# Kernel optimization log

Measured on AMD Instinct MI355X. Metric: run time of the kernel, lower is better.

Reference implementation:

```python
import jax, jax.numpy as jnp
import numpy as np

IN_CAPS, IN_DIMS = 32, 288
OUT_CAPS, OUT_DIMS = 10, 16
N_ITERS = 3


def setup_inputs() -> dict:
    key = jax.random.key(0)
    k1, k2 = jax.random.split(key)
    B = 8192
    data = jax.random.normal(k1, (B, IN_CAPS, IN_DIMS), dtype=jnp.float32)
    stdv = 1.0 / 32.0
    W = jax.random.uniform(k2, (IN_CAPS, IN_DIMS, OUT_CAPS * OUT_DIMS),
                           dtype=jnp.float32, minval=-stdv, maxval=stdv)
    return {"data": data, "W": W}


def reference(data, W):
    B = data.shape[0]
    # u_hat[b,i,o,d]: per-input-capsule predictions for each output capsule
    u_hat = jnp.einsum('bci,cio->bco', data, W).reshape(B, IN_CAPS, OUT_CAPS, OUT_DIMS)
    b = jnp.zeros((IN_CAPS, OUT_CAPS), dtype=u_hat.dtype)
    v = None
    for _ in range(N_ITERS):  # fixed small iteration count
        c = jax.nn.softmax(b, axis=0)                      # (IN_CAPS, OUT_CAPS), softmax over input capsules
        v = jnp.einsum('io,biod->bod', c, u_hat)           # (B, OUT_CAPS, OUT_DIMS)
        # agreement: sqrt of sum of squared elementwise products, averaged over batch
        a = jnp.sqrt(jnp.sum((u_hat * v[:, None, :, :]) ** 2, axis=-1)).mean(axis=0)
        b = b + a
    return v
```

## Files before the change

### kernel.cpp

```cpp
#include <hip/hip_runtime.h>
#include <hip/hip_bf16.h>

#define NB 8192
#define IC 32
#define ID 288
#define OD16 160

typedef __attribute__((ext_vector_type(8))) short bf16x8;
typedef __attribute__((ext_vector_type(4))) float f32x4;

__device__ __forceinline__ unsigned short f2bf(float f) {
    unsigned int u = __builtin_bit_cast(unsigned int, f);
    u = u + 0x7fffu + ((u >> 16) & 1u);
    return (unsigned short)(u >> 16);
}
__device__ __forceinline__ float bf2f(unsigned short h) {
    return __builtin_bit_cast(float, ((unsigned int)h) << 16);
}
__device__ __forceinline__ bf16x8 cvt_bf8(const float4& a, const float4& b) {
    union { __hip_bfloat162 h[4]; bf16x8 v; } u;
    u.h[0] = __float22bfloat162_rn(make_float2(a.x, a.y));
    u.h[1] = __float22bfloat162_rn(make_float2(a.z, a.w));
    u.h[2] = __float22bfloat162_rn(make_float2(b.x, b.y));
    u.h[3] = __float22bfloat162_rn(make_float2(b.z, b.w));
    return u.v;
}

__device__ __forceinline__ void gld_lds16(const void* g, void* l) {
    __builtin_amdgcn_global_load_lds((const __attribute__((address_space(1))) unsigned int*)g,
                                     (__attribute__((address_space(3))) unsigned int*)l, 16, 0, 0);
}

__global__ __launch_bounds__(256) void prep_kernel(const float* __restrict__ W,
                                                   unsigned short* __restrict__ WtImg,
                                                   float* __restrict__ a_arr) {
    __shared__ short tile[160 * 72];
    const int bx = blockIdx.x;
    const int c = bx / 5;
    const int s = bx - c * 5;
    const int t = threadIdx.x;
    if (bx == 0) {
        for (int i = t; i < 3 * 8 * 320; i += 256) a_arr[i] = 0.f;
    }
    const int kw = (s == 4) ? 32 : 64;
    const int nel = kw * 160;
    for (int idx = t; idx < nel; idx += 256) {
        int k = idx / 160;
        int n = idx - k * 160;
        tile[n * 72 + k] = (short)f2bf(W[((long)c * ID + s * 64 + k) * OD16 + n]);
    }
    __syncthreads();
    unsigned short* dst = WtImg + ((long)c * 5 + s) * 10240;
    for (int p = t; p < 1280; p += 256) {
        int n = p >> 3;
        int g = (p & 7) ^ (n & 7);
        uint4 val = make_uint4(0u, 0u, 0u, 0u);
        if (g * 8 < kw) val = *(const uint4*)&tile[n * 72 + g * 8];
        *(uint4*)(dst + p * 8) = val;
    }
}

__global__ __launch_bounds__(256) void gemm_kernel(const float* __restrict__ data,
                                                   const unsigned short* __restrict__ WtImg,
                                                   unsigned short* __restrict__ uhat) {
    __shared__ alignas(16) char Bb[2][20480];
    const int tid = threadIdx.x;
    const int lane = tid & 63;
    const int w = tid >> 6;
    const int q = lane >> 4;
    const int r = lane & 15;
    const int b0 = blockIdx.x * 128;
    const int cc = blockIdx.y;

    const float* A0 = data + (long)(b0 + w * 32 + r) * (IC * ID) + cc * ID;
    const float* A1 = A0 + 16 * (IC * ID);
    const unsigned short* Wc = WtImg + (long)cc * 51200;

    f32x4 acc[2][10];
    #pragma unroll
    for (int i = 0; i < 2; ++i)
        #pragma unroll
        for (int j = 0; j < 10; ++j)
            acc[i][j] = (f32x4){0.f, 0.f, 0.f, 0.f};

    float4 av[2][2][2][2];

    auto issueB = [&](int buf, int s) {
        const unsigned short* src = Wc + s * 10240 + (w * 5) * 512 + lane * 8;
        char* dst = &Bb[buf][(w * 5) * 1024];
        #pragma unroll
        for (int j = 0; j < 5; ++j)
            gld_lds16(src + j * 512, dst + j * 1024);
    };

#define ISSUEA(BANK, S, NKC)                                                   \
    {                                                                          \
        _Pragma("unroll")                                                      \
        for (int kc = 0; kc < (NKC); ++kc) {                                   \
            const int k = (S) * 64 + kc * 32 + q * 8;                          \
            av[BANK][0][kc][0] = *(const float4*)(A0 + k);                     \
            av[BANK][0][kc][1] = *(const float4*)(A0 + k + 4);                 \
            av[BANK][1][kc][0] = *(const float4*)(A1 + k);                     \
            av[BANK][1][kc][1] = *(const float4*)(A1 + k + 4);                 \
        }                                                                      \
    }

#define COMPUTE(BANK, CUR, NKC)                                                \
    {                                                                          \
        _Pragma("unroll")                                                      \
        for (int kc = 0; kc < (NKC); ++kc) {                                   \
            const int kb = kc * 64 + q * 16;                                   \
            bf16x8 bfr[10];                                                    \
            _Pragma("unroll")                                                  \
            for (int nf = 0; nf < 10; ++nf) {                                  \
                const int n = nf * 16 + r;                                     \
                bfr[nf] = *(const bf16x8*)(&Bb[CUR][(n * 128 + kb) ^ ((n & 7) << 4)]); \
            }                                                                  \
            bf16x8 af0 = cvt_bf8(av[BANK][0][kc][0], av[BANK][0][kc][1]);      \
            bf16x8 af1 = cvt_bf8(av[BANK][1][kc][0], av[BANK][1][kc][1]);      \
            _Pragma("unroll")                                                  \
            for (int nf = 0; nf < 10; ++nf) {                                  \
                acc[0][nf] = __builtin_amdgcn_mfma_f32_16x16x32_bf16(af0, bfr[nf], acc[0][nf], 0, 0, 0); \
                acc[1][nf] = __builtin_amdgcn_mfma_f32_16x16x32_bf16(af1, bfr[nf], acc[1][nf], 0, 0, 0); \
            }                                                                  \
        }                                                                      \
    }

#define STAGE(S, BANK, CUR, NKC, NKC_NEXT, WAIT)                               \
    {                                                                          \
        if ((S) < 4) { ISSUEA(1 - (BANK), (S) + 1, NKC_NEXT); issueB(1 - (CUR), (S) + 1); } \
        asm volatile("s_waitcnt vmcnt(" WAIT ")" ::: "memory");                \
        __builtin_amdgcn_s_barrier();                                          \
        __builtin_amdgcn_sched_barrier(0);                                     \
        COMPUTE(BANK, CUR, NKC);                                               \
        if ((S) < 4) __builtin_amdgcn_s_barrier();                             \
    }

    ISSUEA(0, 0, 2);
    issueB(0, 0);

    STAGE(0, 0, 0, 2, 2, "13")
    STAGE(1, 1, 1, 2, 2, "13")
    STAGE(2, 0, 0, 2, 2, "13")
    STAGE(3, 1, 1, 2, 1, "9")
    STAGE(4, 0, 0, 1, 0, "0")

#undef STAGE
#undef COMPUTE
#undef ISSUEA

    __syncthreads();
    short* eb = (short*)&Bb[0][0];
    #pragma unroll
    for (int mf = 0; mf < 2; ++mf)
        #pragma unroll
        for (int rr = 0; rr < 4; ++rr) {
            const int m = w * 32 + mf * 16 + (q << 2) + rr;
            #pragma unroll
            for (int nf = 0; nf < 10; ++nf)
                eb[m * 160 + nf * 16 + r] = (short)f2bf(acc[mf][nf][rr]);
        }
    __syncthreads();
    unsigned short* dstc = uhat + ((long)cc * NB + b0) * 160;
    #pragma unroll
    for (int j = 0; j < 10; ++j) {
        const int chunk = j * 256 + tid;
        *(uint4*)(dstc + chunk * 8) = *(const uint4*)(eb + chunk * 8);
    }
}

template <int COMPUTE_A, int WRITE_V>
__global__ __launch_bounds__(256) void route_kernel(const unsigned short* __restrict__ uhat,
                                                    const float* __restrict__ a_all,
                                                    int n_prev,
                                                    float* __restrict__ a_out,
                                                    float* __restrict__ v_out) {
    constexpr long PL = (long)NB * 160;
    __shared__ float c_sh[320];
    __shared__ float v_lds[4][160];
    __shared__ float a_sh[4][320];
    const int tid = threadIdx.x;
    for (int base = 0; base < 320; base += 256) {
        int t = base + tid;
        if (t < 320) {
            float bv = 0.f;
            for (int j = 0; j < n_prev * 8; ++j) bv += a_all[j * 320 + t];
            bv *= (1.0f / 8192.0f);
            float m = bv;
            #pragma unroll
            for (int off = 1; off < 32; off <<= 1) m = fmaxf(m, __shfl_xor(m, off));
            float e = __expf(bv - m);
            float ssum = e;
            #pragma unroll
            for (int off = 1; off < 32; off <<= 1) ssum += __shfl_xor(ssum, off);
            c_sh[t] = e / ssum;
        }
    }
    __syncthreads();

    const int w = tid >> 6;
    const int lane = tid & 63;
    const long row = (long)blockIdx.x * 4 + w;
    const unsigned short* __restrict__ u = uhat + row * 160;

    ushort4 ua[5][4];
    if (COMPUTE_A) {
        #pragma unroll
        for (int s5 = 0; s5 < 5; ++s5) {
            const int i = lane & 31;
            const int oo = (lane >> 5) + 2 * s5;
            #pragma unroll
            for (int d4 = 0; d4 < 4; ++d4)
                ua[s5][d4] = *(const ushort4*)(u + (long)i * PL + oo * 16 + d4 * 4);
        }
    }

    if (lane < 40) {
        const int q = lane;
        const int o = q >> 2;
        float4 sv = {0.f, 0.f, 0.f, 0.f};
        #pragma unroll 8
        for (int i = 0; i < 32; ++i) {
            ushort4 uu = *(const ushort4*)(u + (long)i * PL + q * 4);
            float ci = c_sh[o * 32 + i];
            sv.x += ci * bf2f(uu.x);
            sv.y += ci * bf2f(uu.y);
            sv.z += ci * bf2f(uu.z);
            sv.w += ci * bf2f(uu.w);
        }
        if (WRITE_V) *(float4*)(v_out + row * 160 + q * 4) = sv;
        if (COMPUTE_A) *(float4*)(&v_lds[w][q * 4]) = sv;
    }

    if (COMPUTE_A) {
        asm volatile("s_waitcnt lgkmcnt(0)" ::: "memory");
        #pragma unroll
        for (int s5 = 0; s5 < 5; ++s5) {
            const int i = lane & 31;
            const int oo = (lane >> 5) + 2 * s5;
            const float* vp = &v_lds[w][oo * 16];
            float accv = 0.f;
            #pragma unroll
            for (int d4 = 0; d4 < 4; ++d4) {
                ushort4 uu = ua[s5][d4];
                float4 vv = *(const float4*)(vp + d4 * 4);
                float p0 = bf2f(uu.x) * vv.x;
                float p1 = bf2f(uu.y) * vv.y;
                float p2 = bf2f(uu.z) * vv.z;
                float p3 = bf2f(uu.w) * vv.w;
                accv += p0 * p0 + p1 * p1 + p2 * p2 + p3 * p3;
            }
            a_sh[w][oo * 32 + i] = sqrtf(accv);
        }
        __syncthreads();
        for (int t = tid; t < 320; t += 256) {
            float s4 = a_sh[0][t] + a_sh[1][t] + a_sh[2][t] + a_sh[3][t];
            atomicAdd(a_out + (blockIdx.x & 7) * 320 + t, s4);
        }
    }
}

extern "C" void kernel_launch(void* const* d_in, const int* in_sizes, int n_in,
                              void* d_out, int out_size, void* d_ws, size_t ws_size,
                              hipStream_t stream) {
    const float* data = (const float*)d_in[0];
    const float* W = (const float*)d_in[1];
    float* out = (float*)d_out;
    char* ws = (char*)d_ws;

    unsigned short* uhat = (unsigned short*)ws;
    size_t off = (size_t)NB * IC * OD16 * 2;
    unsigned short* WtImg = (unsigned short*)(ws + off);
    off += 32L * 5 * 10240 * 2;
    float* a_arr = (float*)(ws + off); off += 3 * 8 * 320 * 4;

    hipLaunchKernelGGL(prep_kernel, dim3(160), dim3(256), 0, stream, W, WtImg, a_arr);
    hipLaunchKernelGGL(gemm_kernel, dim3(64, 32), dim3(256), 0, stream, data, WtImg, uhat);
    hipLaunchKernelGGL((route_kernel<1, 0>), dim3(2048), dim3(256), 0, stream,
                       uhat, a_arr, 0, a_arr + 0 * 2560, out);
    hipLaunchKernelGGL((route_kernel<1, 0>), dim3(2048), dim3(256), 0, stream,
                       uhat, a_arr, 1, a_arr + 1 * 2560, out);
    hipLaunchKernelGGL((route_kernel<0, 1>), dim3(2048), dim3(256), 0, stream,
                       uhat, a_arr, 2, a_arr + 2 * 2560, out);
}
```

Baseline: 194.2 us.

## Stage A operand through LDS via async global_load_lds with swizzled layout

The fp32 activation tile (A) now goes through LDS with async global_load_lds, using an XOR-swizzled layout per wave, instead of being loaded into registers. The main loop is restructured into nine k-chunk computes, with separate double buffering for A and B and hand-placed vmcnt waits and barriers. The aim is to cut register pressure from the register prefetch and to overlap global loads more deeply with MFMA work. In exchange, LDS use grows to 72KB per block, which can lower occupancy, and each k-chunk adds extra LDS reads.

```diff
diff --git a/kernel.cpp b/kernel.cpp
--- a/kernel.cpp
+++ b/kernel.cpp
@@ -17,12 +17,12 @@
 __device__ __forceinline__ float bf2f(unsigned short h) {
     return __builtin_bit_cast(float, ((unsigned int)h) << 16);
 }
-__device__ __forceinline__ bf16x8 cvt_bf8(const float4& a, const float4& b) {
+__device__ __forceinline__ bf16x8 cvt_bf8(const f32x4& a, const f32x4& b) {
     union { __hip_bfloat162 h[4]; bf16x8 v; } u;
-    u.h[0] = __float22bfloat162_rn(make_float2(a.x, a.y));
-    u.h[1] = __float22bfloat162_rn(make_float2(a.z, a.w));
-    u.h[2] = __float22bfloat162_rn(make_float2(b.x, b.y));
-    u.h[3] = __float22bfloat162_rn(make_float2(b.z, b.w));
+    u.h[0] = __float22bfloat162_rn(make_float2(a[0], a[1]));
+    u.h[1] = __float22bfloat162_rn(make_float2(a[2], a[3]));
+    u.h[2] = __float22bfloat162_rn(make_float2(b[0], b[1]));
+    u.h[3] = __float22bfloat162_rn(make_float2(b[2], b[3]));
     return u.v;
 }
 
@@ -63,7 +63,9 @@
 __global__ __launch_bounds__(256) void gemm_kernel(const float* __restrict__ data,
                                                    const unsigned short* __restrict__ WtImg,
                                                    unsigned short* __restrict__ uhat) {
-    __shared__ alignas(16) char Bb[2][20480];
+    __shared__ alignas(16) char lds[73728];
+    char* const Alds = lds;
+    char* const Blds = lds + 32768;
     const int tid = threadIdx.x;
     const int lane = tid & 63;
     const int w = tid >> 6;
@@ -72,8 +74,8 @@
     const int b0 = blockIdx.x * 128;
     const int cc = blockIdx.y;
 
-    const float* A0 = data + (long)(b0 + w * 32 + r) * (IC * ID) + cc * ID;
-    const float* A1 = A0 + 16 * (IC * ID);
+    const float* Ag = data + (long)(b0 + w * 32 + (lane >> 3)) * (IC * ID) + cc * ID
+                      + ((lane & 7) ^ ((lane >> 3) & 7)) * 4;
     const unsigned short* Wc = WtImg + (long)cc * 51200;
 
     f32x4 acc[2][10];
@@ -83,74 +85,70 @@
         for (int j = 0; j < 10; ++j)
             acc[i][j] = (f32x4){0.f, 0.f, 0.f, 0.f};
 
-    float4 av[2][2][2][2];
-
+    auto issueA = [&](int buf, int kc) {
+        char* dst = Alds + w * 8192 + buf * 4096;
+        const float* src = Ag + kc * 32;
+        #pragma unroll
+        for (int j = 0; j < 4; ++j)
+            gld_lds16(src + (long)j * 8 * (IC * ID), dst + j * 1024);
+    };
     auto issueB = [&](int buf, int s) {
         const unsigned short* src = Wc + s * 10240 + (w * 5) * 512 + lane * 8;
-        char* dst = &Bb[buf][(w * 5) * 1024];
+        char* dst = Blds + buf * 20480 + (w * 5) * 1024;
         #pragma unroll
         for (int j = 0; j < 5; ++j)
             gld_lds16(src + j * 512, dst + j * 1024);
     };
 
-#define ISSUEA(BANK, S, NKC)                                                   \
+#define COMPUTE(KC)                                                            \
     {                                                                          \
+        const char* Ab = Alds + w * 8192 + ((KC) & 1) * 4096;                  \
+        const char* Bb = Blds + (((KC) >> 1) & 1) * 20480;                     \
+        const int kb = ((KC) & 1) * 64 + q * 16;                               \
+        bf16x8 bfr[10];                                                        \
         _Pragma("unroll")                                                      \
-        for (int kc = 0; kc < (NKC); ++kc) {                                   \
-            const int k = (S) * 64 + kc * 32 + q * 8;                          \
-            av[BANK][0][kc][0] = *(const float4*)(A0 + k);                     \
-            av[BANK][0][kc][1] = *(const float4*)(A0 + k + 4);                 \
-            av[BANK][1][kc][0] = *(const float4*)(A1 + k);                     \
-            av[BANK][1][kc][1] = *(const float4*)(A1 + k + 4);                 \
+        for (int nf = 0; nf < 10; ++nf) {                                      \
+            const int n = nf * 16 + r;                                         \
+            bfr[nf] = *(const bf16x8*)(Bb + ((n * 128 + kb) ^ ((n & 7) << 4)));\
         }                                                                      \
-    }
-
-#define COMPUTE(BANK, CUR, NKC)                                                \
-    {                                                                          \
+        bf16x8 af[2];                                                          \
         _Pragma("unroll")                                                      \
-        for (int kc = 0; kc < (NKC); ++kc) {                                   \
-            const int kb = kc * 64 + q * 16;                                   \
-            bf16x8 bfr[10];                                                    \
-            _Pragma("unroll")                                                  \
-            for (int nf = 0; nf < 10; ++nf) {                                  \
-                const int n = nf * 16 + r;                                     \
-                bfr[nf] = *(const bf16x8*)(&Bb[CUR][(n * 128 + kb) ^ ((n & 7) << 4)]); \
-            }                                                                  \
-            bf16x8 af0 = cvt_bf8(av[BANK][0][kc][0], av[BANK][0][kc][1]);      \
-            bf16x8 af1 = cvt_bf8(av[BANK][1][kc][0], av[BANK][1][kc][1]);      \
-            _Pragma("unroll")                                                  \
-            for (int nf = 0; nf < 10; ++nf) {                                  \
-                acc[0][nf] = __builtin_amdgcn_mfma_f32_16x16x32_bf16(af0, bfr[nf], acc[0][nf], 0, 0, 0); \
-                acc[1][nf] = __builtin_amdgcn_mfma_f32_16x16x32_bf16(af1, bfr[nf], acc[1][nf], 0, 0, 0); \
-            }                                                                  \
+        for (int mf = 0; mf < 2; ++mf) {                                       \
+            const int row = mf * 16 + r;                                       \
+            const int c0 = (q * 2) ^ (r & 7);                                  \
+            const int c1 = (q * 2 + 1) ^ (r & 7);                              \
+            f32x4 alo = *(const f32x4*)(Ab + row * 128 + c0 * 16);             \
+            f32x4 ahi = *(const f32x4*)(Ab + row * 128 + c1 * 16);             \
+            af[mf] = cvt_bf8(alo, ahi);                                        \
         }                                                                      \
-    }
-
-#define STAGE(S, BANK, CUR, NKC, NKC_NEXT, WAIT)                               \
-    {                                                                          \
-        if ((S) < 4) { ISSUEA(1 - (BANK), (S) + 1, NKC_NEXT); issueB(1 - (CUR), (S) + 1); } \
-        asm volatile("s_waitcnt vmcnt(" WAIT ")" ::: "memory");                \
-        __builtin_amdgcn_s_barrier();                                          \
-        __builtin_amdgcn_sched_barrier(0);                                     \
-        COMPUTE(BANK, CUR, NKC);                                               \
-        if ((S) < 4) __builtin_amdgcn_s_barrier();                             \
-    }
-
-    ISSUEA(0, 0, 2);
-    issueB(0, 0);
-
-    STAGE(0, 0, 0, 2, 2, "13")
-    STAGE(1, 1, 1, 2, 2, "13")
-    STAGE(2, 0, 0, 2, 2, "13")
-    STAGE(3, 1, 1, 2, 1, "9")
-    STAGE(4, 0, 0, 1, 0, "0")
-
-#undef STAGE
+        _Pragma("unroll")                                                      \
+        for (int nf = 0; nf < 10; ++nf) {                                      \
+            acc[0][nf] = __builtin_amdgcn_mfma_f32_16x16x32_bf16(af[0], bfr[nf], acc[0][nf], 0, 0, 0); \
+            acc[1][nf] = __builtin_amdgcn_mfma_f32_16x16x32_bf16(af[1], bfr[nf], acc[1][nf], 0, 0, 0); \
+        }                                                                      \
+    }
+
+#define WAITV(N)  { asm volatile("s_waitcnt vmcnt(" N ")" ::: "memory");       \
+                    __builtin_amdgcn_sched_barrier(0); }
+#define BAR()     { __builtin_amdgcn_s_barrier(); }
+
+    issueA(0, 0); issueB(0, 0); issueA(1, 1); issueB(1, 1);
+    WAITV("9") BAR() COMPUTE(0)
+    issueA(0, 2); WAITV("9") COMPUTE(1) BAR()
+    issueA(1, 3); issueB(0, 2); WAITV("9") BAR() COMPUTE(2)
+    issueA(0, 4); WAITV("9") COMPUTE(3) BAR()
+    issueA(1, 5); issueB(1, 3); WAITV("9") BAR() COMPUTE(4)
+    issueA(0, 6); WAITV("9") COMPUTE(5) BAR()
+    issueA(1, 7); issueB(0, 4); WAITV("9") BAR() COMPUTE(6)
+    issueA(0, 8); WAITV("9") COMPUTE(7) BAR()
+    WAITV("0") BAR() COMPUTE(8)
+
 #undef COMPUTE
-#undef ISSUEA
-
-    __syncthreads();
-    short* eb = (short*)&Bb[0][0];
+#undef WAITV
+#undef BAR
+
+    __syncthreads();
+    short* eb = (short*)Blds;
     #pragma unroll
     for (int mf = 0; mf < 2; ++mf)
         #pragma unroll
```

Measured after the change: 165.5 us. 14.8% less time.
